# Optimization experiments

Hardware: AMD Instinct MI355X
Metric: run time of the kernel (lower is better)

Reference implementation:

```python
import jax, jax.numpy as jnp
import numpy as np
from jax import lax

B, L, M, H = 8, 16, 256, 53
HID, NH, HD = 64, 4, 16  # hidden_size, n_heads, head_dim
ACT = 15  # 3 sub-actions x 5 categories


def _lstm_last(x, Wih, Whh, bih, bhh):
    # x: [N, T, D] batch_first; torch LSTM gate order i,f,g,o. Returns last hidden [N, HID].
    N = x.shape[0]
    h0 = jnp.zeros((N, HID), x.dtype)
    c0 = jnp.zeros((N, HID), x.dtype)
    def step(carry, xt):
        h, c = carry
        g = xt @ Wih.T + bih + h @ Whh.T + bhh
        i, f, gg, o = jnp.split(g, 4, axis=-1)
        c = jax.nn.sigmoid(f) * c + jax.nn.sigmoid(i) * jnp.tanh(gg)
        h = jax.nn.sigmoid(o) * jnp.tanh(c)
        return (h, c), None
    (h, _), _ = lax.scan(step, (h0, c0), x.transpose(1, 0, 2))
    return h


def setup_inputs():
    key = jax.random.key(0)
    ks = jax.random.split(key, 32)
    rn = lambda k, sh: (jax.random.normal(k, sh, jnp.float32) * 0.05)
    Gmat = jax.random.randint(ks[3], (M, M), 0, 2)
    Gmat = Gmat.at[jnp.arange(M), jnp.arange(M)].set(1)  # self-contact so no all-masked row
    return {
        'x_actor': jax.random.normal(ks[0], (B, L, M, H), jnp.float32),
        'x_critic': jax.random.normal(ks[1], (B, L, M, H), jnp.float32),
        'action': jax.random.randint(ks[2], (B, M, 3), 0, 5),
        'Gmat': Gmat,
        'Wa': rn(ks[4], (HID, H)), 'ba': jnp.zeros((HID,), jnp.float32),
        'Wg': rn(ks[5], (HID, H)), 'bg': jnp.zeros((HID,), jnp.float32),
        'Qw': rn(ks[6], (HID, HID)), 'Kw': rn(ks[7], (HID, HID)),
        'W2': rn(ks[8], (HID, 2 * HID)), 'b2': jnp.zeros((HID,), jnp.float32),
        'Wih_a': rn(ks[9], (4 * HID, HID)), 'Whh_a': rn(ks[10], (4 * HID, HID)),
        'bih_a': jnp.zeros((4 * HID,), jnp.float32), 'bhh_a': jnp.zeros((4 * HID,), jnp.float32),
        'Wih_c': rn(ks[11], (4 * HID, HID)), 'Whh_c': rn(ks[12], (4 * HID, HID)),
        'bih_c': jnp.zeros((4 * HID,), jnp.float32), 'bhh_c': jnp.zeros((4 * HID,), jnp.float32),
        'Wma1': rn(ks[13], (HID, HID)), 'bma1': jnp.zeros((HID,), jnp.float32),
        'Wma2': rn(ks[14], (ACT, HID)), 'bma2': jnp.zeros((ACT,), jnp.float32),
        'Wmc1': rn(ks[15], (HID, HID)), 'bmc1': jnp.zeros((HID,), jnp.float32),
        'Wmc2': rn(ks[16], (1, HID)), 'bmc2': jnp.zeros((1,), jnp.float32),
    }


def reference(x_actor, x_critic, action, Gmat, Wa, ba, Wg, bg, Qw, Kw, W2, b2,
              Wih_a, Whh_a, bih_a, bhh_a, Wih_c, Whh_c, bih_c, bhh_c,
              Wma1, bma1, Wma2, bma2, Wmc1, bmc1, Wmc2, bmc2):
    Bb, Ll, Mm, Hh = x_actor.shape
    xa = x_actor.transpose(1, 0, 2, 3).reshape(Ll * Bb, Mm, Hh)
    xc = xa  # original code overwrites x_critic with x_actor (preserved)
    a_lin = xa @ Wa.T + ba                               # [LB, M, HID]
    # --- GAT (GCN2) ---
    s = xc @ Wg.T + bg                                   # [LB, M, HID]
    q = (s @ Qw).reshape(-1, Mm, NH, HD)
    k = (s @ Kw).reshape(-1, Mm, NH, HD)
    s4 = s.reshape(-1, Mm, NH, HD)
    att = jnp.einsum('blhe,bshe->bhls', q, k) / jnp.asarray(128.0, s.dtype) ** 0.5
    att = jnp.where(Gmat > 0, att, jnp.asarray(-9e15, att.dtype))
    att = jax.nn.softmax(att, axis=-1)
    s_out = jnp.einsum('bshe,bhls->blhe', s4, att).reshape(-1, Mm, NH * HD)
    c_feat = jnp.concatenate([s, s_out], axis=-1) @ W2.T + b2  # [LB, M, HID]
    # --- to sequences [B*M, L, HID] ---
    xa_seq = a_lin.reshape(Ll, Bb * Mm, HID).transpose(1, 0, 2)
    xc_seq = c_feat.reshape(Ll, Bb * Mm, HID).transpose(1, 0, 2)
    ah = _lstm_last(xa_seq, Wih_a, Whh_a, bih_a, bhh_a)          # [B*M, HID]
    ch = _lstm_last(xc_seq, Wih_c, Whh_c, bih_c, bhh_c).reshape(Bb, Mm, HID)
    logits = (jnp.tanh(ah @ Wma1.T + bma1) @ Wma2.T + bma2).reshape(Bb, Mm, 3, 5)
    logp = jax.nn.log_softmax(logits, axis=-1)
    lp = jnp.take_along_axis(logp, action[..., None], axis=-1).squeeze(-1)  # [B,M,3]
    ent = -jnp.sum(jnp.exp(logp) * logp, axis=-1)                           # [B,M,3]
    value = jnp.tanh(ch @ Wmc1.T + bmc1) @ Wmc2.T + bmc2                    # [B,M,1]
    return (action, lp.sum(-1), ent.sum(-1), value)
```

## Files before the change

### kernel.cpp

```cpp
#include <hip/hip_runtime.h>
#include <math.h>

#define B_ 8
#define L_ 16
#define M_ 256
#define H_ 53
#define HID_ 64
#define LB_ 128
#define SCALE_ 0.08838834764831845f

typedef __attribute__((ext_vector_type(8))) short bf16x8;
typedef __attribute__((ext_vector_type(4))) float f32x4;

__device__ inline unsigned short f2bf(float f) {
  unsigned u = __builtin_bit_cast(unsigned, f);
  unsigned r = (u + 0x7FFFu + ((u >> 16) & 1u)) >> 16;
  return (unsigned short)r;
}
__device__ inline float bf2f(unsigned short u) {
  unsigned v = ((unsigned)u) << 16;
  return __builtin_bit_cast(float, v);
}
__device__ inline float sigm(float x) { return __builtin_amdgcn_rcpf(1.f + __expf(-x)); }
__device__ inline float ftanh(float x) { return 1.f - 2.f * __builtin_amdgcn_rcpf(1.f + __expf(2.f * x)); }

__global__ __launch_bounds__(256) void kP_pre(
    const float* __restrict__ Wa, const float* __restrict__ Wg,
    const float* __restrict__ bg,
    const float* __restrict__ Qw, const float* __restrict__ Kw,
    const int* __restrict__ Gmat, const float* __restrict__ Wih_c,
    const float* __restrict__ W2, const float* __restrict__ b2,
    const float* __restrict__ Whh_a, const float* __restrict__ Whh_c,
    const float* __restrict__ Wih_a,
    unsigned short* __restrict__ WQ_b, unsigned short* __restrict__ WK_b,
    float* __restrict__ bqk, unsigned short* __restrict__ Wfold_b,
    float* __restrict__ bias_fold, unsigned* __restrict__ gmask,
    unsigned short* __restrict__ Whha_b, unsigned short* __restrict__ Whhc_b,
    unsigned short* __restrict__ Wiha_b, unsigned short* __restrict__ Wab_b) {
  int blk = blockIdx.x, tid = threadIdx.x;
  if (blk < 32) {
    int idx = blk * 256 + tid;
    int which = idx >> 12, n = (idx >> 6) & 63, j = idx & 63;
    const float* Mm = which ? Kw : Qw;
    float acc = 0.f;
    if (j < 53) {
      for (int e = 0; e < 64; ++e) acc = fmaf(Mm[e * 64 + n], Wg[e * 53 + j], acc);
      if (which == 0) acc *= SCALE_;
    }
    (which ? WK_b : WQ_b)[n * 64 + j] = f2bf(acc);
  } else if (blk == 32) {
    if (tid < 128) {
      int which = tid >> 6, n = tid & 63;
      const float* Mm = which ? Kw : Qw;
      float acc = 0.f;
      for (int e = 0; e < 64; ++e) acc = fmaf(bg[e], Mm[e * 64 + n], acc);
      if (which == 0) acc *= SCALE_;
      bqk[tid] = acc;
    }
    float bacc = 0.f;
    for (int e = 0; e < 64; ++e) bacc = fmaf(Wih_c[tid * 64 + e], b2[e], bacc);
    bias_fold[tid] = bacc;
  } else if (blk < 97) {
    int l = (blk - 33) * 4 + (tid >> 6);
    int ln = tid & 63;
    #pragma unroll
    for (int c = 0; c < 4; ++c) {
      int gv = Gmat[l * 256 + c * 64 + ln];
      unsigned long long msk = __ballot(gv > 0);
      if (ln == 0) {
        gmask[l * 8 + c * 2] = (unsigned)msk;
        gmask[l * 8 + c * 2 + 1] = (unsigned)(msk >> 32);
      }
    }
  } else if (blk < 225) {
    int idx = (blk - 97) * 256 + tid;
    int n = idx >> 7, t = idx & 127;
    float acc = 0.f;
    for (int e = 0; e < 64; ++e) acc = fmaf(Wih_c[n * 64 + e], W2[e * 128 + t], acc);
    Wfold_b[idx] = f2bf(acc);
  } else if (blk < 249) {
    int base = (blk - 225) * 2048;
    #pragma unroll
    for (int k = 0; k < 8; ++k) {
      int idx = base + k * 256 + tid;
      if (idx < 16384) Whha_b[idx] = f2bf(Whh_a[idx]);
      else if (idx < 32768) Whhc_b[idx - 16384] = f2bf(Whh_c[idx - 16384]);
      else Wiha_b[idx - 32768] = f2bf(Wih_a[idx - 32768]);
    }
  } else {
    int base = (blk - 249) * 4096;
    #pragma unroll
    for (int k = 0; k < 16; ++k) {
      int idx = base + k * 256 + tid;
      int n = idx >> 6, j = idx & 63;
      float v = 0.f;
      if (j < 53) v = (n < 64) ? Wa[n * 53 + j] : Wg[(n - 64) * 53 + j];
      Wab_b[idx] = f2bf(v);
    }
  }
}

#define WS 68
#define OS 268
__global__ __launch_bounds__(256, 2) void kA_lin(const float* __restrict__ x,
    const unsigned short* __restrict__ Wab_b,
    const unsigned short* __restrict__ WQ_b, const unsigned short* __restrict__ WK_b,
    const float* __restrict__ ba, const float* __restrict__ bg,
    const float* __restrict__ bqk,
    unsigned short* __restrict__ a_lin_bf, unsigned short* __restrict__ s_b,
    unsigned short* __restrict__ q_b, unsigned short* __restrict__ k_b,
    unsigned short* __restrict__ sT_b) {
  __shared__ __attribute__((aligned(16))) char smem[70144];
  float* x_raw = (float*)smem;
  unsigned short* out_lds = (unsigned short*)smem;
  unsigned short* w_lds = (unsigned short*)(smem + 34304);
  float* bias_lds = (float*)(smem + 69120);
  int tid = threadIdx.x, blk = blockIdx.x;
  int row0 = blk * 64;
  int lbA = row0 >> 8, m0 = row0 & 255;
  int lA = lbA >> 3, bA = lbA & 7;
  {
    const uint4* xs = (const uint4*)(x + ((bA * L_ + lA) * M_ + m0) * H_);
    uint4* xr = (uint4*)x_raw;
    #pragma unroll
    for (int k = 0; k < 4; ++k) {
      int i = k * 256 + tid;
      if (i < 848) xr[i] = xs[i];
    }
  }
  #pragma unroll
  for (int k = 0; k < 8; ++k) {
    int i = k * 256 + tid;
    int n = i >> 3, c8 = (i & 7) * 8;
    const unsigned short* src = n < 128 ? Wab_b + n * 64
                              : (n < 192 ? WQ_b + (n - 128) * 64 : WK_b + (n - 192) * 64);
    *(uint4*)&w_lds[n * WS + c8] = *(const uint4*)(src + c8);
  }
  {
    float bv;
    if (tid < 64) bv = ba[tid];
    else if (tid < 128) bv = bg[tid - 64];
    else bv = bqk[tid - 128];
    bias_lds[tid] = bv;
  }
  __syncthreads();
  int lane = tid & 63, w = tid >> 6;
  int c16 = lane & 15, q4 = lane >> 4;
  int lrow = w * 16 + c16;
  bf16x8 a0, a1;
  #pragma unroll
  for (int e = 0; e < 8; ++e)
    a0[e] = (short)f2bf(x_raw[lrow * H_ + q4 * 8 + e]);
  #pragma unroll
  for (int e = 0; e < 8; ++e) {
    int c = 32 + q4 * 8 + e;
    a1[e] = (c < H_) ? (short)f2bf(x_raw[lrow * H_ + c]) : (short)0;
  }
  __syncthreads();
  #pragma unroll
  for (int nt = 0; nt < 16; ++nt) {
    bf16x8 b0 = *(const bf16x8*)&w_lds[(nt * 16 + c16) * WS + q4 * 8];
    bf16x8 b1 = *(const bf16x8*)&w_lds[(nt * 16 + c16) * WS + 32 + q4 * 8];
    float bs = bias_lds[nt * 16 + c16];
    f32x4 acc = {bs, bs, bs, bs};
    acc = __builtin_amdgcn_mfma_f32_16x16x32_bf16(a0, b0, acc, 0, 0, 0);
    acc = __builtin_amdgcn_mfma_f32_16x16x32_bf16(a1, b1, acc, 0, 0, 0);
    #pragma unroll
    for (int rr = 0; rr < 4; ++rr)
      out_lds[(w * 16 + q4 * 4 + rr) * OS + nt * 16 + c16] = f2bf(acc[rr]);
  }
  __syncthreads();
  #pragma unroll
  for (int k = 0; k < 8; ++k) {
    int i = k * 256 + tid;
    int r = i >> 5, seg = i & 31;
    int which = seg >> 3, n8 = (seg & 7) * 8;
    uint4 v = *(const uint4*)&out_lds[r * OS + which * 64 + n8];
    unsigned short* dst = which == 0 ? a_lin_bf : which == 1 ? s_b : which == 2 ? q_b : k_b;
    *(uint4*)&dst[(row0 + r) * 64 + n8] = v;
  }
  #pragma unroll
  for (int k = 0; k < 4; ++k) {
    int i = k * 256 + tid;
    int e = i >> 4, mc = i & 15;
    ushort4 v;
    v.x = out_lds[(mc * 4 + 0) * OS + 64 + e];
    v.y = out_lds[(mc * 4 + 1) * OS + 64 + e];
    v.z = out_lds[(mc * 4 + 2) * OS + 64 + e];
    v.w = out_lds[(mc * 4 + 3) * OS + 64 + e];
    *(ushort4*)&sT_b[(lbA * 64 + e) * 256 + m0 + mc * 4] = v;
  }
}

__global__ __launch_bounds__(512, 4) void kB_attn(
    const unsigned short* __restrict__ qb, const unsigned short* __restrict__ kb,
    const unsigned short* __restrict__ sT, const unsigned* __restrict__ gmask,
    unsigned short* __restrict__ so_b) {
  __shared__ __attribute__((aligned(16))) unsigned short k_lds[256 * 68];
  __shared__ __attribute__((aligned(16))) unsigned short sT_lds[64 * 280];
  int blk = blockIdx.x;
  int lb = blk >> 2;
  int l0 = (blk & 3) << 6;
  int tid = threadIdx.x;
  int kbase = lb * 256;
  for (int i = tid; i < 2048; i += 512) {
    int s = i >> 3, e8 = (i & 7) * 8;
    *(uint4*)&k_lds[s * 68 + e8] = *(const uint4*)(kb + (kbase + s) * 64 + e8);
  }
  for (int i = tid; i < 2048; i += 512) {
    int e = i >> 5, m8 = (i & 31) * 8;
    *(uint4*)&sT_lds[e * 280 + m8] = *(const uint4*)(sT + (lb * 64 + e) * 256 + m8);
  }
  int lane = tid & 63, w = tid >> 6;
  int c16 = lane & 15, q4 = lane >> 4;
  int lrow0 = (w >> 1) * 16;
  int h0 = (w & 1) * 2;
  int lrow = lb * 256 + l0 + lrow0;
  const bf16x8 z8 = {0, 0, 0, 0, 0, 0, 0, 0};
  bf16x8 bq[2];
  #pragma unroll
  for (int hp = 0; hp < 2; ++hp) {
    int h = h0 + hp;
    bq[hp] = (q4 < 2) ? *(const bf16x8*)(qb + (lrow + c16) * 64 + h * 16 + q4 * 8) : z8;
  }
  unsigned gwv[8];
  #pragma unroll
  for (int sp = 0; sp < 8; ++sp) gwv[sp] = gmask[(l0 + lrow0 + c16) * 8 + sp];
  __syncthreads();
  f32x4 accO[2];
  float sumh[2];
  #pragma unroll
  for (int hp = 0; hp < 2; ++hp) { accO[hp] = (f32x4){0.f, 0.f, 0.f, 0.f}; sumh[hp] = 0.f; }

  #pragma unroll
  for (int sp = 0; sp < 8; ++sp) {
    unsigned gw = gwv[sp];
    #pragma unroll
    for (int hp = 0; hp < 2; ++hp) {
      int h = h0 + hp;
      unsigned pk0A, pk1A, pk0B, pk1B;
      #pragma unroll
      for (int tp = 0; tp < 2; ++tp) {
        int t = sp * 2 + tp;
        bf16x8 ka = z8;
        if (q4 < 2) ka = *(const bf16x8*)&k_lds[(t * 16 + c16) * 68 + h * 16 + q4 * 8];
        f32x4 d = __builtin_amdgcn_mfma_f32_16x16x32_bf16(ka, bq[hp], (f32x4){0.f, 0.f, 0.f, 0.f}, 0, 0, 0);
        int bitbase = tp * 16 + q4 * 4;
        float p0 = ((gw >> (bitbase + 0)) & 1u) ? __expf(d[0]) : 0.f;
        float p1 = ((gw >> (bitbase + 1)) & 1u) ? __expf(d[1]) : 0.f;
        float p2 = ((gw >> (bitbase + 2)) & 1u) ? __expf(d[2]) : 0.f;
        float p3 = ((gw >> (bitbase + 3)) & 1u) ? __expf(d[3]) : 0.f;
        sumh[hp] += (p0 + p1) + (p2 + p3);
        unsigned lo = (unsigned)f2bf(p0) | ((unsigned)f2bf(p1) << 16);
        unsigned hi = (unsigned)f2bf(p2) | ((unsigned)f2bf(p3) << 16);
        if (tp == 0) { pk0A = lo; pk1A = hi; } else { pk0B = lo; pk1B = hi; }
      }
      int srcA = ((q4 & 1) * 2) * 16 + c16, srcB = srcA + 16;
      unsigned g0A = (unsigned)__shfl((int)pk0A, srcA);
      unsigned g1A = (unsigned)__shfl((int)pk1A, srcA);
      unsigned g2A = (unsigned)__shfl((int)pk0A, srcB);
      unsigned g3A = (unsigned)__shfl((int)pk1A, srcB);
      unsigned g0B = (unsigned)__shfl((int)pk0B, srcA);
      unsigned g1B = (unsigned)__shfl((int)pk1B, srcA);
      unsigned g2B = (unsigned)__shfl((int)pk0B, srcB);
      unsigned g3B = (unsigned)__shfl((int)pk1B, srcB);
      bool useB = (q4 >= 2);
      uint4 av;
      av.x = useB ? g0B : g0A;
      av.y = useB ? g1B : g1A;
      av.z = useB ? g2B : g2A;
      av.w = useB ? g3B : g3A;
      bf16x8 af = __builtin_bit_cast(bf16x8, av);
      bf16x8 bs = *(const bf16x8*)&sT_lds[(h * 16 + c16) * 280 + sp * 32 + q4 * 8];
      accO[hp] = __builtin_amdgcn_mfma_f32_16x16x32_bf16(af, bs, accO[hp], 0, 0, 0);
    }
  }
  #pragma unroll
  for (int hp = 0; hp < 2; ++hp) {
    int h = h0 + hp;
    float s = sumh[hp];
    s += __shfl_xor(s, 16);
    s += __shfl_xor(s, 32);
    #pragma unroll
    for (int r = 0; r < 4; ++r) {
      float sv = __shfl(s, q4 * 4 + r);
      float o = accO[hp][r] / sv;
      so_b[(lb * 256 + l0 + lrow0 + q4 * 4 + r) * 64 + h * 16 + c16] = f2bf(o);
    }
  }
}

__global__ __launch_bounds__(256, 1) void kR_lstm(
    const unsigned short* __restrict__ a_lin_bf,
    const unsigned short* __restrict__ s_b, const unsigned short* __restrict__ so_b,
    const unsigned short* __restrict__ Wfold_b, const float* __restrict__ bias_fold,
    const unsigned short* __restrict__ Wiha_b,
    const unsigned short* __restrict__ Whha_b, const unsigned short* __restrict__ Whhc_b,
    const float* __restrict__ bih_a, const float* __restrict__ bhh_a,
    const float* __restrict__ bih_c, const float* __restrict__ bhh_c,
    const int* __restrict__ action,
    const float* __restrict__ Wma1, const float* __restrict__ bma1,
    const float* __restrict__ Wma2, const float* __restrict__ bma2,
    const float* __restrict__ Wmc1, const float* __restrict__ bmc1,
    const float* __restrict__ Wmc2, const float* __restrict__ bmc2,
    float* __restrict__ out) {
  int blk = blockIdx.x;
  int which = blk >> 7, g = blk & 127;
  int seq0 = g * 16;
  int b = seq0 >> 8, m0 = seq0 & 255;
  __shared__ __attribute__((aligned(16))) unsigned short h_lds[2][16][72];
  __shared__ __attribute__((aligned(16))) unsigned short ha_lds[16][72];
  __shared__ float logit_lds[16][16];
  __shared__ float grp_lds[16][8];
  __shared__ float val_lds[16][4];
  int tid = threadIdx.x;
  int lane = tid & 63, w = tid >> 6;
  int c16 = lane & 15, q4 = lane >> 4;
  int hs0 = w * 16;
  const unsigned short* Whh_b = which ? Whhc_b : Whha_b;
  const float* bih = which ? bih_c : bih_a;
  const float* bhh = which ? bhh_c : bhh_a;
  bf16x8 bwhh[4][2];
  float bias[4];
  #pragma unroll
  for (int nt = 0; nt < 4; ++nt) {
    int n = nt * 64 + hs0 + c16;
    bias[nt] = bih[n] + bhh[n] + (which ? bias_fold[n] : 0.f);
    #pragma unroll
    for (int kf = 0; kf < 2; ++kf)
      bwhh[nt][kf] = *(const bf16x8*)(Whh_b + n * 64 + kf * 32 + q4 * 8);
  }
  for (int i = tid; i < 576; i += 256) ((unsigned*)h_lds)[i] = 0u;
  float cr[4] = {0.f, 0.f, 0.f, 0.f};
  const int STEP = 2048 * 64;
  __syncthreads();
  int cur = 0;
  if (which == 0) {
    bf16x8 bwin[4][2];
    #pragma unroll
    for (int nt = 0; nt < 4; ++nt) {
      int n = nt * 64 + hs0 + c16;
      #pragma unroll
      for (int kf = 0; kf < 2; ++kf)
        bwin[nt][kf] = *(const bf16x8*)(Wiha_b + n * 64 + kf * 32 + q4 * 8);
    }
    const unsigned short* inb = a_lin_bf + (b * 256 + m0 + c16) * 64;
    bf16x8 i0c = *(const bf16x8*)(inb + q4 * 8);
    bf16x8 i1c = *(const bf16x8*)(inb + 32 + q4 * 8);
    for (int l = 0; l < L_; ++l) {
      bf16x8 i0n = i0c, i1n = i1c;
      if (l < L_ - 1) {
        i0n = *(const bf16x8*)(inb + (l + 1) * STEP + q4 * 8);
        i1n = *(const bf16x8*)(inb + (l + 1) * STEP + 32 + q4 * 8);
      }
      bf16x8 ah0 = *(const bf16x8*)&h_lds[cur][c16][q4 * 8];
      bf16x8 ah1 = *(const bf16x8*)&h_lds[cur][c16][32 + q4 * 8];
      f32x4 acc[4];
      #pragma unroll
      for (int nt = 0; nt < 4; ++nt) {
        f32x4 a = {bias[nt], bias[nt], bias[nt], bias[nt]};
        a = __builtin_amdgcn_mfma_f32_16x16x32_bf16(i0c, bwin[nt][0], a, 0, 0, 0);
        a = __builtin_amdgcn_mfma_f32_16x16x32_bf16(i1c, bwin[nt][1], a, 0, 0, 0);
        a = __builtin_amdgcn_mfma_f32_16x16x32_bf16(ah0, bwhh[nt][0], a, 0, 0, 0);
        a = __builtin_amdgcn_mfma_f32_16x16x32_bf16(ah1, bwhh[nt][1], a, 0, 0, 0);
        acc[nt] = a;
      }
      #pragma unroll
      for (int rr = 0; rr < 4; ++rr) {
        float si = sigm(acc[0][rr]);
        float sf = sigm(acc[1][rr]);
        float gg = ftanh(acc[2][rr]);
        float so_ = sigm(acc[3][rr]);
        cr[rr] = sf * cr[rr] + si * gg;
        float hvv = so_ * ftanh(cr[rr]);
        h_lds[cur ^ 1][q4 * 4 + rr][hs0 + c16] = f2bf(hvv);
      }
      __syncthreads();
      cur ^= 1;
      i0c = i0n; i1c = i1n;
    }
  } else {
    bf16x8 bwf[4][4];
    #pragma unroll
    for (int nt = 0; nt < 4; ++nt) {
      int n = nt * 64 + hs0 + c16;
      #pragma unroll
      for (int kc = 0; kc < 4; ++kc)
        bwf[nt][kc] = *(const bf16x8*)(Wfold_b + n * 128 + kc * 32 + q4 * 8);
    }
    const unsigned short* sbB = s_b + (b * 256 + m0 + c16) * 64;
    const unsigned short* soB = so_b + (b * 256 + m0 + c16) * 64;
    bf16x8 s0c = *(const bf16x8*)(sbB + q4 * 8);
    bf16x8 s1c = *(const bf16x8*)(sbB + 32 + q4 * 8);
    bf16x8 o0c = *(const bf16x8*)(soB + q4 * 8);
    bf16x8 o1c = *(const bf16x8*)(soB + 32 + q4 * 8);
    for (int l = 0; l < L_; ++l) {
      bf16x8 s0n = s0c, s1n = s1c, o0n = o0c, o1n = o1c;
      if (l < L_ - 1) {
        s0n = *(const bf16x8*)(sbB + (l + 1) * STEP + q4 * 8);
        s1n = *(const bf16x8*)(sbB + (l + 1) * STEP + 32 + q4 * 8);
        o0n = *(const bf16x8*)(soB + (l + 1) * STEP + q4 * 8);
        o1n = *(const bf16x8*)(soB + (l + 1) * STEP + 32 + q4 * 8);
      }
      bf16x8 ah0 = *(const bf16x8*)&h_lds[cur][c16][q4 * 8];
      bf16x8 ah1 = *(const bf16x8*)&h_lds[cur][c16][32 + q4 * 8];
      f32x4 acc[4];
      #pragma unroll
      for (int nt = 0; nt < 4; ++nt) {
        f32x4 a = {bias[nt], bias[nt], bias[nt], bias[nt]};
        a = __builtin_amdgcn_mfma_f32_16x16x32_bf16(s0c, bwf[nt][0], a, 0, 0, 0);
        a = __builtin_amdgcn_mfma_f32_16x16x32_bf16(s1c, bwf[nt][1], a, 0, 0, 0);
        a = __builtin_amdgcn_mfma_f32_16x16x32_bf16(o0c, bwf[nt][2], a, 0, 0, 0);
        a = __builtin_amdgcn_mfma_f32_16x16x32_bf16(o1c, bwf[nt][3], a, 0, 0, 0);
        a = __builtin_amdgcn_mfma_f32_16x16x32_bf16(ah0, bwhh[nt][0], a, 0, 0, 0);
        a = __builtin_amdgcn_mfma_f32_16x16x32_bf16(ah1, bwhh[nt][1], a, 0, 0, 0);
        acc[nt] = a;
      }
      #pragma unroll
      for (int rr = 0; rr < 4; ++rr) {
        float si = sigm(acc[0][rr]);
        float sf = sigm(acc[1][rr]);
        float gg = ftanh(acc[2][rr]);
        float so_ = sigm(acc[3][rr]);
        cr[rr] = sf * cr[rr] + si * gg;
        float hvv = so_ * ftanh(cr[rr]);
        h_lds[cur ^ 1][q4 * 4 + rr][hs0 + c16] = f2bf(hvv);
      }
      __syncthreads();
      cur ^= 1;
      s0c = s0n; s1c = s1n; o0c = o0n; o1c = o1n;
    }
  }
  bf16x8 fh0 = *(const bf16x8*)&h_lds[cur][c16][q4 * 8];
  bf16x8 fh1 = *(const bf16x8*)&h_lds[cur][c16][32 + q4 * 8];
  if (which == 0) {
    bf16x8 bm1[2];
    #pragma unroll
    for (int kf = 0; kf < 2; ++kf) {
      const float* wp = Wma1 + (hs0 + c16) * 64 + kf * 32 + q4 * 8;
      bf16x8 bb;
      #pragma unroll
      for (int j = 0; j < 8; ++j) bb[j] = (short)f2bf(wp[j]);
      bm1[kf] = bb;
    }
    float bs = bma1[hs0 + c16];
    f32x4 acc = {bs, bs, bs, bs};
    acc = __builtin_amdgcn_mfma_f32_16x16x32_bf16(fh0, bm1[0], acc, 0, 0, 0);
    acc = __builtin_amdgcn_mfma_f32_16x16x32_bf16(fh1, bm1[1], acc, 0, 0, 0);
    #pragma unroll
    for (int rr = 0; rr < 4; ++rr)
      ha_lds[q4 * 4 + rr][hs0 + c16] = f2bf(ftanh(acc[rr]));
    __syncthreads();
    if (w == 0) {
      bf16x8 af0 = *(const bf16x8*)&ha_lds[c16][q4 * 8];
      bf16x8 af1 = *(const bf16x8*)&ha_lds[c16][32 + q4 * 8];
      const bf16x8 z8 = {0, 0, 0, 0, 0, 0, 0, 0};
      bf16x8 bw2[2] = {z8, z8};
      float bs2 = 0.f;
      if (c16 < 15) {
        #pragma unroll
        for (int kf = 0; kf < 2; ++kf) {
          const float* wp = Wma2 + c16 * 64 + kf * 32 + q4 * 8;
          bf16x8 bb;
          #pragma unroll
          for (int j = 0; j < 8; ++j) bb[j] = (short)f2bf(wp[j]);
          bw2[kf] = bb;
        }
        bs2 = bma2[c16];
      }
      f32x4 acc2 = {bs2, bs2, bs2, bs2};
      acc2 = __builtin_amdgcn_mfma_f32_16x16x32_bf16(af0, bw2[0], acc2, 0, 0, 0);
      acc2 = __builtin_amdgcn_mfma_f32_16x16x32_bf16(af1, bw2[1], acc2, 0, 0, 0);
      #pragma unroll
      for (int rr = 0; rr < 4; ++rr)
        logit_lds[q4 * 4 + rr][c16] = acc2[rr];
    }
    __syncthreads();
    if (tid < 48) {
      int useq = tid & 15, t = tid >> 4;
      int n = seq0 + useq;
      float l0 = logit_lds[useq][t * 5 + 0], l1 = logit_lds[useq][t * 5 + 1];
      float l2 = logit_lds[useq][t * 5 + 2], l3 = logit_lds[useq][t * 5 + 3];
      float l4 = logit_lds[useq][t * 5 + 4];
      float mx = fmaxf(fmaxf(fmaxf(l0, l1), fmaxf(l2, l3)), l4);
      float sm = __expf(l0 - mx) + __expf(l1 - mx) + __expf(l2 - mx) +
                 __expf(l3 - mx) + __expf(l4 - mx);
      float lse = __logf(sm) + mx;
      int a = action[n * 3 + t];
      float lp0 = l0 - lse, lp1 = l1 - lse, lp2 = l2 - lse, lp3 = l3 - lse, lp4 = l4 - lse;
      float lpsel = logit_lds[useq][t * 5 + a] - lse;
      float ent = -(__expf(lp0) * lp0 + __expf(lp1) * lp1 + __expf(lp2) * lp2 +
                    __expf(lp3) * lp3 + __expf(lp4) * lp4);
      grp_lds[useq][t] = lpsel;
      grp_lds[useq][4 + t] = ent;
      out[n * 3 + t] = (float)a;
    }
    __syncthreads();
    if (tid < 16) {
      int n = seq0 + tid;
      out[6144 + n] = grp_lds[tid][0] + grp_lds[tid][1] + grp_lds[tid][2];
      out[8192 + n] = grp_lds[tid][4] + grp_lds[tid][5] + grp_lds[tid][6];
    }
  } else {
    bf16x8 bm1[2];
    #pragma unroll
    for (int kf = 0; kf < 2; ++kf) {
      const float* wp = Wmc1 + (hs0 + c16) * 64 + kf * 32 + q4 * 8;
      bf16x8 bb;
      #pragma unroll
      for (int j = 0; j < 8; ++j) bb[j] = (short)f2bf(wp[j]);
      bm1[kf] = bb;
    }
    float bs = bmc1[hs0 + c16];
    f32x4 acc = {bs, bs, bs, bs};
    acc = __builtin_amdgcn_mfma_f32_16x16x32_bf16(fh0, bm1[0], acc, 0, 0, 0);
    acc = __builtin_amdgcn_mfma_f32_16x16x32_bf16(fh1, bm1[1], acc, 0, 0, 0);
    float wv2 = Wmc2[hs0 + c16];
    float pv[4];
    #pragma unroll
    for (int rr = 0; rr < 4; ++rr) pv[rr] = ftanh(acc[rr]) * wv2;
    #pragma unroll
    for (int rr = 0; rr < 4; ++rr) {
      pv[rr] += __shfl_xor(pv[rr], 1);
      pv[rr] += __shfl_xor(pv[rr], 2);
      pv[rr] += __shfl_xor(pv[rr], 4);
      pv[rr] += __shfl_xor(pv[rr], 8);
    }
    if (c16 == 0) {
      #pragma unroll
      for (int rr = 0; rr < 4; ++rr) val_lds[q4 * 4 + rr][w] = pv[rr];
    }
    __syncthreads();
    if (tid < 16) {
      int n = seq0 + tid;
      out[10240 + n] = val_lds[tid][0] + val_lds[tid][1] + val_lds[tid][2] +
                       val_lds[tid][3] + bmc2[0];
    }
  }
}

extern "C" void kernel_launch(void* const* d_in, const int* in_sizes, int n_in,
                              void* d_out, int out_size, void* d_ws, size_t ws_size,
                              hipStream_t stream) {
  const float* x_actor = (const float*)d_in[0];
  const int* action = (const int*)d_in[2];
  const int* Gmat  = (const int*)d_in[3];
  const float* Wa = (const float*)d_in[4];  const float* ba = (const float*)d_in[5];
  const float* Wg = (const float*)d_in[6];  const float* bg = (const float*)d_in[7];
  const float* Qw = (const float*)d_in[8];  const float* Kw = (const float*)d_in[9];
  const float* W2 = (const float*)d_in[10]; const float* b2 = (const float*)d_in[11];
  const float* Wih_a = (const float*)d_in[12]; const float* Whh_a = (const float*)d_in[13];
  const float* bih_a = (const float*)d_in[14]; const float* bhh_a = (const float*)d_in[15];
  const float* Wih_c = (const float*)d_in[16]; const float* Whh_c = (const float*)d_in[17];
  const float* bih_c = (const float*)d_in[18]; const float* bhh_c = (const float*)d_in[19];
  const float* Wma1 = (const float*)d_in[20]; const float* bma1 = (const float*)d_in[21];
  const float* Wma2 = (const float*)d_in[22]; const float* bma2 = (const float*)d_in[23];
  const float* Wmc1 = (const float*)d_in[24]; const float* bmc1 = (const float*)d_in[25];
  const float* Wmc2 = (const float*)d_in[26]; const float* bmc2 = (const float*)d_in[27];

  unsigned short* us = (unsigned short*)d_ws;
  unsigned short* a_lin_bf = us;
  unsigned short* s_b  = us + 2097152;
  unsigned short* q_b  = us + 4194304;
  unsigned short* k_b  = us + 6291456;
  unsigned short* sT_b = us + 8388608;
  unsigned short* so_b = us + 10485760;
  unsigned short* Wfold_b = us + 12582912;
  unsigned short* Whha_b  = us + 12615680;
  unsigned short* Whhc_b  = us + 12632064;
  unsigned short* Wiha_b  = us + 12648448;
  unsigned short* WQ_b    = us + 12664832;
  unsigned short* WK_b    = us + 12668928;
  unsigned short* Wab_b   = us + 12673024;
  float* fb = (float*)(us + 12681216);
  float* bias_fold = fb;
  float* bqk = fb + 256;
  unsigned* gmask = (unsigned*)(fb + 384);
  float* out = (float*)d_out;

  kP_pre<<<251, 256, 0, stream>>>(Wa, Wg, bg, Qw, Kw, Gmat, Wih_c, W2, b2,
                                  Whh_a, Whh_c, Wih_a,
                                  WQ_b, WK_b, bqk, Wfold_b, bias_fold, gmask,
                                  Whha_b, Whhc_b, Wiha_b, Wab_b);
  kA_lin<<<512, 256, 0, stream>>>(x_actor, Wab_b, WQ_b, WK_b, ba, bg, bqk,
                                  a_lin_bf, s_b, q_b, k_b, sT_b);
  kB_attn<<<512, 512, 0, stream>>>(q_b, k_b, sT_b, gmask, so_b);
  kR_lstm<<<256, 256, 0, stream>>>(a_lin_bf, s_b, so_b, Wfold_b, bias_fold,
                                   Wiha_b, Whha_b, Whhc_b,
                                   bih_a, bhh_a, bih_c, bhh_c,
                                   action, Wma1, bma1, Wma2, bma2,
                                   Wmc1, bmc1, Wmc2, bmc2, out);
}
```

Measured before the change: 68.59 us.

## Move independent weight prep into kA_lin grid and swizzle attention blocks by XCD

The weight-fold, mask-ballot, bias-fold and LSTM weight conversion work that kB/kR need but kA does not is moved out of the prep kernel into extra blocks appended to the kA_lin grid. This shrinks the serial prep kernel and lets that work overlap with the linear projection. kB_attn's block index is also remapped so that blocks sharing the same lb land on the same XCD, improving L2 reuse of k and sT tiles. The extra blocks declare no LDS but share the kernel's LDS allocation and launch bounds.

```diff
diff --git a/kernel.cpp b/kernel.cpp
--- a/kernel.cpp
+++ b/kernel.cpp
@@ -28,15 +28,8 @@
     const float* __restrict__ Wa, const float* __restrict__ Wg,
     const float* __restrict__ bg,
     const float* __restrict__ Qw, const float* __restrict__ Kw,
-    const int* __restrict__ Gmat, const float* __restrict__ Wih_c,
-    const float* __restrict__ W2, const float* __restrict__ b2,
-    const float* __restrict__ Whh_a, const float* __restrict__ Whh_c,
-    const float* __restrict__ Wih_a,
     unsigned short* __restrict__ WQ_b, unsigned short* __restrict__ WK_b,
-    float* __restrict__ bqk, unsigned short* __restrict__ Wfold_b,
-    float* __restrict__ bias_fold, unsigned* __restrict__ gmask,
-    unsigned short* __restrict__ Whha_b, unsigned short* __restrict__ Whhc_b,
-    unsigned short* __restrict__ Wiha_b, unsigned short* __restrict__ Wab_b) {
+    float* __restrict__ bqk, unsigned short* __restrict__ Wab_b) {
   int blk = blockIdx.x, tid = threadIdx.x;
   if (blk < 32) {
     int idx = blk * 256 + tid;
@@ -57,38 +50,8 @@
       if (which == 0) acc *= SCALE_;
       bqk[tid] = acc;
     }
-    float bacc = 0.f;
-    for (int e = 0; e < 64; ++e) bacc = fmaf(Wih_c[tid * 64 + e], b2[e], bacc);
-    bias_fold[tid] = bacc;
-  } else if (blk < 97) {
-    int l = (blk - 33) * 4 + (tid >> 6);
-    int ln = tid & 63;
-    #pragma unroll
-    for (int c = 0; c < 4; ++c) {
-      int gv = Gmat[l * 256 + c * 64 + ln];
-      unsigned long long msk = __ballot(gv > 0);
-      if (ln == 0) {
-        gmask[l * 8 + c * 2] = (unsigned)msk;
-        gmask[l * 8 + c * 2 + 1] = (unsigned)(msk >> 32);
-      }
-    }
-  } else if (blk < 225) {
-    int idx = (blk - 97) * 256 + tid;
-    int n = idx >> 7, t = idx & 127;
-    float acc = 0.f;
-    for (int e = 0; e < 64; ++e) acc = fmaf(Wih_c[n * 64 + e], W2[e * 128 + t], acc);
-    Wfold_b[idx] = f2bf(acc);
-  } else if (blk < 249) {
-    int base = (blk - 225) * 2048;
-    #pragma unroll
-    for (int k = 0; k < 8; ++k) {
-      int idx = base + k * 256 + tid;
-      if (idx < 16384) Whha_b[idx] = f2bf(Whh_a[idx]);
-      else if (idx < 32768) Whhc_b[idx - 16384] = f2bf(Whh_c[idx - 16384]);
-      else Wiha_b[idx - 32768] = f2bf(Wih_a[idx - 32768]);
-    }
   } else {
-    int base = (blk - 249) * 4096;
+    int base = (blk - 33) * 4096;
     #pragma unroll
     for (int k = 0; k < 16; ++k) {
       int idx = base + k * 256 + tid;
@@ -107,15 +70,59 @@
     const unsigned short* __restrict__ WQ_b, const unsigned short* __restrict__ WK_b,
     const float* __restrict__ ba, const float* __restrict__ bg,
     const float* __restrict__ bqk,
+    const int* __restrict__ Gmat, const float* __restrict__ Wih_c,
+    const float* __restrict__ W2, const float* __restrict__ b2,
+    const float* __restrict__ Whh_a, const float* __restrict__ Whh_c,
+    const float* __restrict__ Wih_a,
     unsigned short* __restrict__ a_lin_bf, unsigned short* __restrict__ s_b,
     unsigned short* __restrict__ q_b, unsigned short* __restrict__ k_b,
-    unsigned short* __restrict__ sT_b) {
+    unsigned short* __restrict__ sT_b,
+    unsigned short* __restrict__ Wfold_b, float* __restrict__ bias_fold,
+    unsigned* __restrict__ gmask,
+    unsigned short* __restrict__ Whha_b, unsigned short* __restrict__ Whhc_b,
+    unsigned short* __restrict__ Wiha_b) {
+  int tid = threadIdx.x, blk = blockIdx.x;
+  if (blk >= 512) {
+    int b2k = blk - 512;
+    if (b2k < 128) {
+      int idx = b2k * 256 + tid;
+      int n = idx >> 7, t = idx & 127;
+      float acc = 0.f;
+      for (int e = 0; e < 64; ++e) acc = fmaf(Wih_c[n * 64 + e], W2[e * 128 + t], acc);
+      Wfold_b[idx] = f2bf(acc);
+    } else if (b2k < 192) {
+      int l = (b2k - 128) * 4 + (tid >> 6);
+      int ln = tid & 63;
+      #pragma unroll
+      for (int c = 0; c < 4; ++c) {
+        int gv = Gmat[l * 256 + c * 64 + ln];
+        unsigned long long msk = __ballot(gv > 0);
+        if (ln == 0) {
+          gmask[l * 8 + c * 2] = (unsigned)msk;
+          gmask[l * 8 + c * 2 + 1] = (unsigned)(msk >> 32);
+        }
+      }
+    } else if (b2k == 192) {
+      float acc = 0.f;
+      for (int e = 0; e < 64; ++e) acc = fmaf(Wih_c[tid * 64 + e], b2[e], acc);
+      bias_fold[tid] = acc;
+    } else {
+      int base = (b2k - 193) * 2048;
+      #pragma unroll
+      for (int k = 0; k < 8; ++k) {
+        int idx = base + k * 256 + tid;
+        if (idx < 16384) Whha_b[idx] = f2bf(Whh_a[idx]);
+        else if (idx < 32768) Whhc_b[idx - 16384] = f2bf(Whh_c[idx - 16384]);
+        else Wiha_b[idx - 32768] = f2bf(Wih_a[idx - 32768]);
+      }
+    }
+    return;
+  }
   __shared__ __attribute__((aligned(16))) char smem[70144];
   float* x_raw = (float*)smem;
   unsigned short* out_lds = (unsigned short*)smem;
   unsigned short* w_lds = (unsigned short*)(smem + 34304);
   float* bias_lds = (float*)(smem + 69120);
-  int tid = threadIdx.x, blk = blockIdx.x;
   int row0 = blk * 64;
   int lbA = row0 >> 8, m0 = row0 & 255;
   int lA = lbA >> 3, bA = lbA & 7;
@@ -198,9 +205,11 @@
     unsigned short* __restrict__ so_b) {
   __shared__ __attribute__((aligned(16))) unsigned short k_lds[256 * 68];
   __shared__ __attribute__((aligned(16))) unsigned short sT_lds[64 * 280];
-  int blk = blockIdx.x;
-  int lb = blk >> 2;
-  int l0 = (blk & 3) << 6;
+  int bid = blockIdx.x;
+  int xcd = bid & 7;
+  int rest = bid >> 3;
+  int l0 = (rest & 3) << 6;
+  int lb = (rest >> 2) * 8 + xcd;
   int tid = threadIdx.x;
   int kbase = lb * 256;
   for (int i = tid; i < 2048; i += 512) {
@@ -578,12 +587,12 @@
   unsigned* gmask = (unsigned*)(fb + 384);
   float* out = (float*)d_out;
 
-  kP_pre<<<251, 256, 0, stream>>>(Wa, Wg, bg, Qw, Kw, Gmat, Wih_c, W2, b2,
-                                  Whh_a, Whh_c, Wih_a,
-                                  WQ_b, WK_b, bqk, Wfold_b, bias_fold, gmask,
-                                  Whha_b, Whhc_b, Wiha_b, Wab_b);
-  kA_lin<<<512, 256, 0, stream>>>(x_actor, Wab_b, WQ_b, WK_b, ba, bg, bqk,
-                                  a_lin_bf, s_b, q_b, k_b, sT_b);
+  kP_pre<<<35, 256, 0, stream>>>(Wa, Wg, bg, Qw, Kw, WQ_b, WK_b, bqk, Wab_b);
+  kA_lin<<<729, 256, 0, stream>>>(x_actor, Wab_b, WQ_b, WK_b, ba, bg, bqk,
+                                  Gmat, Wih_c, W2, b2, Whh_a, Whh_c, Wih_a,
+                                  a_lin_bf, s_b, q_b, k_b, sT_b,
+                                  Wfold_b, bias_fold, gmask,
+                                  Whha_b, Whhc_b, Wiha_b);
   kB_attn<<<512, 512, 0, stream>>>(q_b, k_b, sT_b, gmask, so_b);
   kR_lstm<<<256, 256, 0, stream>>>(a_lin_bf, s_b, so_b, Wfold_b, bias_fold,
                                    Wiha_b, Whha_b, Whhc_b,
```

Result: no change. 67.94 us (median of 3 runs) (-0.9%).
